# Kernel tuning notes

Measured on AMD Instinct MI355X. Metric: run time of the kernel, lower is better.

## Reference

```python
import jax, jax.numpy as jnp
import numpy as np

N = 100_000      # num nodes
E = 6_400_000    # num edges
P = 12           # periods
F = 32           # output_size (TGCN hidden)


def setup_inputs() -> dict:
    key = jax.random.key(0)
    ks = jax.random.split(key, 16)
    g = lambda i, shape, s=0.1: jax.random.normal(ks[i], shape, dtype=jnp.float32) * s
    zf = jnp.zeros((F,), jnp.float32)
    return {
        "x": jax.random.normal(ks[0], (N, P), dtype=jnp.float32),
        "edge_index": jax.random.randint(ks[1], (2, E), 0, N, dtype=jnp.int64),
        "edge_weight": jax.random.uniform(ks[2], (E,), dtype=jnp.float32),
        "attention": g(3, (P,), 1.0),            # A3TGCN learned period attention
        # GCNConv weights: in_channels=1 -> weight is effectively a length-F vector
        "wc_z": g(4, (F,)), "bc_z": zf,
        "wc_r": g(5, (F,)), "bc_r": zf,
        "wc_h": g(6, (F,)), "bc_h": zf,
        # TGCN gate linears: Linear(2F, F) with bias
        "wl_z": g(7, (2 * F, F)), "bl_z": zf,
        "wl_r": g(8, (2 * F, F)), "bl_r": zf,
        "wl_h": g(9, (2 * F, F)), "bl_h": zf,
        # final Linear(F, 1)
        "w_out": g(10, (F, 1)), "b_out": jnp.zeros((1,), jnp.float32),
    }


def reference(x, edge_index, edge_weight, attention,
              wc_z, bc_z, wc_r, bc_r, wc_h, bc_h,
              wl_z, bl_z, wl_r, bl_r, wl_h, bl_h,
              w_out, b_out):
    n = x.shape[0]
    src, dst = edge_index[0], edge_index[1]

    # GCN normalization with added self-loops (weight 1): D^{-1/2} (A + I) D^{-1/2}
    deg = jax.ops.segment_sum(edge_weight, dst, num_segments=n) + 1.0
    dinv = jax.lax.rsqrt(deg)
    norm = dinv[src] * edge_weight * dinv[dst]          # (E,)

    # GCNConv is linear and in_channels == 1, so conv_g(X_p)_i = agg(X_p)_i * W_g + b_g
    # where agg is the normalized (self-loop augmented) scalar aggregation.
    # Aggregate all periods at once: (E, P) messages -> (N, P)
    agg = jax.ops.segment_sum(norm[:, None] * x[src], dst, num_segments=n)
    agg = agg + (dinv * dinv)[:, None] * x              # self-loop term, (N, P)

    probs = jax.nn.softmax(attention)                   # (P,)
    H0 = jnp.zeros((n, F), x.dtype)                     # A3TGCN calls TGCN with H=None each period
    H_acc = jnp.zeros((n, F), x.dtype)
    for p in range(P):                                  # small fixed structural loop
        s = agg[:, p, None]                             # (N, 1)
        conv_z = s * wc_z + bc_z                        # (N, F)
        conv_r = s * wc_r + bc_r
        conv_h = s * wc_h + bc_h
        Z = jax.nn.sigmoid(jnp.concatenate([conv_z, H0], axis=1) @ wl_z + bl_z)
        R = jax.nn.sigmoid(jnp.concatenate([conv_r, H0], axis=1) @ wl_r + bl_r)
        Ht = jnp.tanh(jnp.concatenate([conv_h, H0 * R], axis=1) @ wl_h + bl_h)
        Hp = Z * H0 + (1.0 - Z) * Ht                    # TGCN single step from zero state
        H_acc = H_acc + probs[p] * Hp

    h = jax.nn.relu(H_acc)
    return h @ w_out + b_out                            # (N, 1)
```

## Files before the change

### kernel.cpp

```cpp
#include <hip/hip_runtime.h>

#define NN 100000
#define EE 6400000
#define PP 12
#define FF 32

#define VV   128
#define BB   782
#define CAP  8832
#define K1B  800
#define CHK  8000
#define AST  13
#define XST  16

__global__ void precompute_k(const float* __restrict__ att,
                             const float* __restrict__ wc_z, const float* __restrict__ bc_z,
                             const float* __restrict__ wc_h, const float* __restrict__ bc_h,
                             const float* __restrict__ wl_z, const float* __restrict__ bl_z,
                             const float* __restrict__ wl_h, const float* __restrict__ bl_h,
                             float* __restrict__ tabs) {
    int j = threadIdx.x;
    if (j < FF) {
        float az = 0.f, cz = 0.f, ah = 0.f, ch = 0.f;
        for (int f = 0; f < FF; ++f) {
            float wz = wl_z[f * FF + j];
            float wh = wl_h[f * FF + j];
            az += wc_z[f] * wz;
            cz += bc_z[f] * wz;
            ah += wc_h[f] * wh;
            ch += bc_h[f] * wh;
        }
        tabs[16 + j]          = az;
        tabs[16 + FF + j]     = cz + bl_z[j];
        tabs[16 + 2 * FF + j] = ah;
        tabs[16 + 3 * FF + j] = ch + bl_h[j];
    } else if (j == FF) {
        float a[PP];
        float m = -1e30f;
        for (int p = 0; p < PP; ++p) { a[p] = att[p]; m = fmaxf(m, a[p]); }
        float s = 0.f;
        for (int p = 0; p < PP; ++p) { a[p] = __expf(a[p] - m); s += a[p]; }
        for (int p = 0; p < PP; ++p) tabs[p] = a[p] / s;
    }
}

__global__ __launch_bounds__(512) void bucket_k(const int* __restrict__ src,
                                                const int* __restrict__ dst,
                                                const float* __restrict__ ew,
                                                int* __restrict__ bucket_cnt,
                                                uint2* __restrict__ recs) {
    __shared__ int hist[BB];
    __shared__ int offs[BB];
    int tid = threadIdx.x;
    int beg = blockIdx.x * CHK;
    int end = beg + CHK;

    for (int b = tid; b < BB; b += 512) hist[b] = 0;
    __syncthreads();

    for (int e = beg + tid; e < end; e += 512)
        atomicAdd(&hist[dst[e] >> 7], 1);
    __syncthreads();

    for (int b = tid; b < BB; b += 512) {
        int h = hist[b];
        offs[b] = h ? atomicAdd(&bucket_cnt[b], h) : 0;
    }
    __syncthreads();

    for (int e = beg + tid; e < end; e += 512) {
        int d = dst[e];
        int bin   = d >> 7;
        int local = d & (VV - 1);
        int o = atomicAdd(&offs[bin], 1);
        if (o < CAP) {
            uint2 r;
            r.x = ((unsigned)local << 17) | (unsigned)src[e];
            r.y = __float_as_uint(ew[e]);
            recs[(size_t)bin * CAP + o] = r;
        }
    }
}

__global__ __launch_bounds__(256) void deg2_k(const int* __restrict__ bucket_cnt,
                                              const uint2* __restrict__ recs,
                                              const float* __restrict__ x,
                                              float* __restrict__ xds) {
    __shared__ unsigned long long wsum[VV];
    int b = blockIdx.x;
    int tid = threadIdx.x;
    if (tid < VV) wsum[tid] = 0ull;
    __syncthreads();

    int n = min(bucket_cnt[b], CAP);
    const uint2* r = recs + (size_t)b * CAP;
    for (int k = tid; k < n; k += 256) {
        uint2 v = r[k];
        unsigned long long w = (unsigned long long)(__uint_as_float(v.y) * 4294967296.0f);
        atomicAdd(&wsum[v.x >> 17], w);
    }
    __syncthreads();

    int node = b * VV + tid;
    if (tid < VV && node < NN) {
        float wf = (float)wsum[tid] * (1.0f / 4294967296.0f);
        float dv = rsqrtf(wf + 1.0f);
        const float4* xr = (const float4*)(x + (size_t)node * PP);
        float4* xo = (float4*)(xds + ((size_t)node << 4));
        #pragma unroll
        for (int q = 0; q < 3; ++q) {
            float4 v = xr[q];
            v.x *= dv; v.y *= dv; v.z *= dv; v.w *= dv;
            xo[q] = v;
        }
        xds[((size_t)node << 4) + 12] = dv;
    }
}

__global__ __launch_bounds__(512) void sortagg_k(const int* __restrict__ bucket_cnt,
                                                 const uint2* __restrict__ recs,
                                                 const float* __restrict__ xds,
                                                 const float* __restrict__ tabs,
                                                 const float* __restrict__ w_out,
                                                 const float* __restrict__ b_out,
                                                 float* __restrict__ out) {
    __shared__ uint2 srec[CAP];
    __shared__ int   h[VV];
    __shared__ int   starts_s[VV];
    __shared__ int   offs[VV];
    __shared__ int   cnts_s[VV];
    __shared__ float agg[VV * AST];
    int b = blockIdx.x;
    int tid = threadIdx.x;

    if (tid < VV) h[tid] = 0;
    __syncthreads();

    int n = min(bucket_cnt[b], CAP);
    const uint2* r = recs + (size_t)b * CAP;

    for (int k = tid; k < n; k += 512)
        atomicAdd(&h[r[k].x >> 17], 1);
    __syncthreads();

    int own = (tid < VV) ? h[tid] : 0;
    #pragma unroll
    for (int off = 1; off < VV; off <<= 1) {
        int t = (tid < VV && tid >= off) ? h[tid - off] : 0;
        __syncthreads();
        if (tid < VV) h[tid] += t;
        __syncthreads();
    }
    if (tid < VV) {
        int pre = h[tid] - own;
        starts_s[tid] = pre;
        offs[tid]     = pre;
        cnts_s[tid]   = own;
    }
    __syncthreads();

    for (int k = tid; k < n; k += 512) {
        uint2 v = r[k];
        int p = atomicAdd(&offs[v.x >> 17], 1);
        srec[p] = v;
    }
    __syncthreads();

    {
        int local = tid >> 2;
        int q     = tid & 3;
        int st = starts_s[local];
        int cn = cnts_s[local];

        float acc[PP];
        #pragma unroll
        for (int p = 0; p < PP; ++p) acc[p] = 0.f;

        for (int m = q; m < cn; m += 4) {
            uint2 v = srec[st + m];
            float c = __uint_as_float(v.y);
            const float4* xs = (const float4*)(xds + ((size_t)(v.x & 0x1FFFFu) << 4));
            float4 v0 = xs[0], v1 = xs[1], v2 = xs[2];
            acc[0] += c * v0.x;  acc[1] += c * v0.y;  acc[2]  += c * v0.z;  acc[3]  += c * v0.w;
            acc[4] += c * v1.x;  acc[5] += c * v1.y;  acc[6]  += c * v1.z;  acc[7]  += c * v1.w;
            acc[8] += c * v2.x;  acc[9] += c * v2.y;  acc[10] += c * v2.z;  acc[11] += c * v2.w;
        }

        #pragma unroll
        for (int p = 0; p < PP; ++p) {
            acc[p] += __shfl_xor(acc[p], 1, 4);
            acc[p] += __shfl_xor(acc[p], 2, 4);
        }
        if (q == 0) {
            float* ap = &agg[local * AST];
            #pragma unroll
            for (int p = 0; p < PP; ++p) ap[p] = acc[p];
        }
    }
    __syncthreads();

    int g = tid >> 5;
    int j = tid & 31;
    float azj = tabs[16 + j];
    float czj = tabs[16 + FF + j];
    float ahj = tabs[16 + 2 * FF + j];
    float chj = tabs[16 + 3 * FF + j];

    for (int nl = g; nl < VV; nl += 16) {
        int i = b * VV + nl;
        if (i >= NN) continue;
        float dv = xds[((size_t)i << 4) + 12];
        const float* ai = &agg[nl * AST];

        float accum = 0.f;
        #pragma unroll
        for (int p = 0; p < PP; ++p) {
            float sp = dv * (ai[p] + xds[((size_t)i << 4) + p]);
            float pr = tabs[p];
            float uz = sp * azj + czj;
            float uh = sp * ahj + chj;
            float one_minus_z = 1.0f / (1.0f + __expf(uz));
            float e2h = __expf(2.0f * uh);
            float th  = 1.0f - 2.0f / (e2h + 1.0f);
            accum += pr * one_minus_z * th;
        }
        float hv = fmaxf(accum, 0.f) * w_out[j];
        #pragma unroll
        for (int off = 16; off > 0; off >>= 1)
            hv += __shfl_xor(hv, off, 32);
        if (j == 0) out[i] = hv + b_out[0];
    }
}

__global__ __launch_bounds__(256) void deg_k(const int* __restrict__ dst,
                                             const float* __restrict__ ew,
                                             float* __restrict__ deg) {
    int stride = gridDim.x * blockDim.x;
    for (int e = blockIdx.x * blockDim.x + threadIdx.x; e < EE; e += stride)
        atomicAdd(&deg[dst[e]], ew[e]);
}

__global__ __launch_bounds__(256) void dinv_self_k(const float* __restrict__ x,
                                                   float* __restrict__ deg,
                                                   float* __restrict__ agg) {
    int i = blockIdx.x * blockDim.x + threadIdx.x;
    if (i >= NN) return;
    float d  = deg[i] + 1.0f;
    float dv = rsqrtf(d);
    deg[i]   = dv;
    float dv2 = dv * dv;
    const float4* xr = (const float4*)(x + (size_t)i * PP);
    float4* ar = (float4*)(agg + (size_t)i * PP);
    #pragma unroll
    for (int q = 0; q < 3; ++q) {
        float4 v = xr[q];
        v.x *= dv2; v.y *= dv2; v.z *= dv2; v.w *= dv2;
        ar[q] = v;
    }
}

__global__ __launch_bounds__(256) void agg_k(const int* __restrict__ src,
                                             const int* __restrict__ dst,
                                             const float* __restrict__ ew,
                                             const float* __restrict__ x,
                                             const float* __restrict__ dinv,
                                             float* __restrict__ agg) {
    int stride = gridDim.x * blockDim.x;
    for (int e = blockIdx.x * blockDim.x + threadIdx.x; e < EE; e += stride) {
        int s = src[e];
        int d = dst[e];
        float nw = dinv[s] * ew[e] * dinv[d];
        const float4* xs = (const float4*)(x + (size_t)s * PP);
        float* ad = agg + (size_t)d * PP;
        float4 v0 = xs[0], v1 = xs[1], v2 = xs[2];
        atomicAdd(&ad[0],  nw * v0.x);
        atomicAdd(&ad[1],  nw * v0.y);
        atomicAdd(&ad[2],  nw * v0.z);
        atomicAdd(&ad[3],  nw * v0.w);
        atomicAdd(&ad[4],  nw * v1.x);
        atomicAdd(&ad[5],  nw * v1.y);
        atomicAdd(&ad[6],  nw * v1.z);
        atomicAdd(&ad[7],  nw * v1.w);
        atomicAdd(&ad[8],  nw * v2.x);
        atomicAdd(&ad[9],  nw * v2.y);
        atomicAdd(&ad[10], nw * v2.z);
        atomicAdd(&ad[11], nw * v2.w);
    }
}

__global__ __launch_bounds__(256) void node_k(const float* __restrict__ agg,
                                              const float* __restrict__ tabs,
                                              const float* __restrict__ w_out,
                                              const float* __restrict__ b_out,
                                              float* __restrict__ out) {
    int t = blockIdx.x * blockDim.x + threadIdx.x;
    int i = t >> 5;
    int j = t & 31;
    if (i >= NN) return;
    float azj = tabs[16 + j];
    float czj = tabs[16 + FF + j];
    float ahj = tabs[16 + 2 * FF + j];
    float chj = tabs[16 + 3 * FF + j];
    float acc = 0.f;
    #pragma unroll
    for (int p = 0; p < PP; ++p) {
        float s  = agg[i * PP + p];
        float pr = tabs[p];
        float uz = s * azj + czj;
        float uh = s * ahj + chj;
        float one_minus_z = 1.0f / (1.0f + __expf(uz));
        float e2h = __expf(2.0f * uh);
        float th  = 1.0f - 2.0f / (e2h + 1.0f);
        acc += pr * one_minus_z * th;
    }
    float h = fmaxf(acc, 0.f) * w_out[j];
    #pragma unroll
    for (int off = 16; off > 0; off >>= 1)
        h += __shfl_xor(h, off, 32);
    if (j == 0) out[i] = h + b_out[0];
}

extern "C" void kernel_launch(void* const* d_in, const int* in_sizes, int n_in,
                              void* d_out, int out_size, void* d_ws, size_t ws_size,
                              hipStream_t stream) {
    const float* x    = (const float*)d_in[0];
    const int*   ei   = (const int*)d_in[1];
    const float* ew   = (const float*)d_in[2];
    const float* att  = (const float*)d_in[3];
    const float* wc_z = (const float*)d_in[4];
    const float* bc_z = (const float*)d_in[5];
    const float* wc_h = (const float*)d_in[8];
    const float* bc_h = (const float*)d_in[9];
    const float* wl_z = (const float*)d_in[10];
    const float* bl_z = (const float*)d_in[11];
    const float* wl_h = (const float*)d_in[14];
    const float* bl_h = (const float*)d_in[15];
    const float* wout = (const float*)d_in[16];
    const float* bout = (const float*)d_in[17];
    float* out = (float*)d_out;

    const int* src = ei;
    const int* dst = ei + EE;

    size_t region  = (size_t)BB * CAP * sizeof(uint2);
    size_t cnt_pad = 3136;
    size_t xds_sz  = (size_t)NN * XST * sizeof(float);
    size_t need    = region + cnt_pad + xds_sz + 4096;

    if (ws_size >= need) {
        uint2* recs       = (uint2*)d_ws;
        int*   bucket_cnt = (int*)((char*)d_ws + region);
        float* xds        = (float*)((char*)d_ws + region + cnt_pad);
        float* tabs       = (float*)((char*)d_ws + region + cnt_pad + xds_sz);

        hipMemsetAsync(bucket_cnt, 0, BB * sizeof(int), stream);
        precompute_k<<<1, 64, 0, stream>>>(att, wc_z, bc_z, wc_h, bc_h, wl_z, bl_z, wl_h, bl_h, tabs);
        bucket_k<<<K1B, 512, 0, stream>>>(src, dst, ew, bucket_cnt, recs);
        deg2_k<<<BB, 256, 0, stream>>>(bucket_cnt, recs, x, xds);
        sortagg_k<<<BB, 512, 0, stream>>>(bucket_cnt, recs, xds, tabs, wout, bout, out);
    } else {
        float* deg  = (float*)d_ws;
        float* agg  = deg + NN;
        float* tabs = agg + (size_t)NN * PP;

        hipMemsetAsync(deg, 0, NN * sizeof(float), stream);
        precompute_k<<<1, 64, 0, stream>>>(att, wc_z, bc_z, wc_h, bc_h, wl_z, bl_z, wl_h, bl_h, tabs);
        deg_k<<<4096, 256, 0, stream>>>(dst, ew, deg);
        dinv_self_k<<<(NN + 255) / 256, 256, 0, stream>>>(x, deg, agg);
        agg_k<<<8192, 256, 0, stream>>>(src, dst, ew, x, deg, agg);
        node_k<<<NN * 32 / 256, 256, 0, stream>>>(agg, tabs, wout, bout, out);
    }
}
```

Before: 420.4 us.

## Sort edge chunks locally in LDS and write contiguously with per-chunk bucket offset table

Each bucketing block now fully sorts its 8000-edge chunk by destination bucket in shared memory and writes it out contiguously, recording per-bucket start offsets in a 16-bit table. This replaces scattered global writes and global atomics on bucket counters. The degree and aggregation kernels then gather each bucket's records from 800 chunk segments using that table, which removes the memset and the capacity-padded region. The cost is fragmented, small-segment reads in the consumer kernels and extra shared memory, and the agg buffer now reuses the srec space.

```diff
diff --git a/kernel.cpp b/kernel.cpp
--- a/kernel.cpp
+++ b/kernel.cpp
@@ -10,6 +10,7 @@
 #define CAP  8832
 #define K1B  800
 #define CHK  8000
+#define NBIN 784
 #define AST  13
 #define XST  16
 
@@ -44,60 +45,87 @@
     }
 }
 
-__global__ __launch_bounds__(512) void bucket_k(const int* __restrict__ src,
-                                                const int* __restrict__ dst,
-                                                const float* __restrict__ ew,
-                                                int* __restrict__ bucket_cnt,
-                                                uint2* __restrict__ recs) {
-    __shared__ int hist[BB];
-    __shared__ int offs[BB];
+__global__ __launch_bounds__(512) void bucketsort_k(const int* __restrict__ src,
+                                                    const int* __restrict__ dst,
+                                                    const float* __restrict__ ew,
+                                                    uint2* __restrict__ recs,
+                                                    unsigned short* __restrict__ T16) {
+    __shared__ uint2 srec[CHK];
+    __shared__ int   hist[NBIN];
+    __shared__ int   offs[NBIN];
     int tid = threadIdx.x;
-    int beg = blockIdx.x * CHK;
-    int end = beg + CHK;
-
-    for (int b = tid; b < BB; b += 512) hist[b] = 0;
-    __syncthreads();
-
-    for (int e = beg + tid; e < end; e += 512)
-        atomicAdd(&hist[dst[e] >> 7], 1);
-    __syncthreads();
-
-    for (int b = tid; b < BB; b += 512) {
-        int h = hist[b];
-        offs[b] = h ? atomicAdd(&bucket_cnt[b], h) : 0;
-    }
-    __syncthreads();
-
-    for (int e = beg + tid; e < end; e += 512) {
-        int d = dst[e];
-        int bin   = d >> 7;
-        int local = d & (VV - 1);
-        int o = atomicAdd(&offs[bin], 1);
-        if (o < CAP) {
-            uint2 r;
-            r.x = ((unsigned)local << 17) | (unsigned)src[e];
-            r.y = __float_as_uint(ew[e]);
-            recs[(size_t)bin * CAP + o] = r;
-        }
-    }
-}
-
-__global__ __launch_bounds__(256) void deg2_k(const int* __restrict__ bucket_cnt,
-                                              const uint2* __restrict__ recs,
+    int blk = blockIdx.x;
+    int beg = blk * CHK;
+
+    for (int b = tid; b < NBIN; b += 512) hist[b] = 0;
+    __syncthreads();
+
+    for (int e = tid; e < CHK; e += 512)
+        atomicAdd(&hist[dst[beg + e] >> 7], 1);
+    __syncthreads();
+
+    int i2   = 512 + tid;
+    int own0 = hist[tid];
+    int own1 = (i2 < NBIN) ? hist[i2] : 0;
+    for (int off = 1; off < NBIN; off <<= 1) {
+        int a0 = (tid >= off) ? hist[tid - off] : 0;
+        int a1 = (i2 < NBIN) ? hist[i2 - off] : 0;
+        __syncthreads();
+        hist[tid] += a0;
+        if (i2 < NBIN) hist[i2] += a1;
+        __syncthreads();
+    }
+    offs[tid] = hist[tid] - own0;
+    if (i2 < NBIN) offs[i2] = hist[i2] - own1;
+    __syncthreads();
+
+    for (int b = tid; b < 783; b += 512)
+        T16[(size_t)b * K1B + blk] = (unsigned short)offs[b];
+    __syncthreads();
+
+    for (int e = tid; e < CHK; e += 512) {
+        int ee = beg + e;
+        int d  = dst[ee];
+        uint2 r;
+        r.x = ((unsigned)(d & (VV - 1)) << 17) | (unsigned)src[ee];
+        r.y = __float_as_uint(ew[ee]);
+        int p = atomicAdd(&offs[d >> 7], 1);
+        srec[p] = r;
+    }
+    __syncthreads();
+
+    uint2* o = recs + (size_t)blk * CHK;
+    for (int k = tid; k < CHK; k += 512)
+        o[k] = srec[k];
+}
+
+__global__ __launch_bounds__(512) void deg2_k(const uint2* __restrict__ recs,
+                                              const unsigned short* __restrict__ T16,
                                               const float* __restrict__ x,
                                               float* __restrict__ xds) {
     __shared__ unsigned long long wsum[VV];
+    __shared__ int rstart[K1B], rcnt[K1B];
     int b = blockIdx.x;
     int tid = threadIdx.x;
+
     if (tid < VV) wsum[tid] = 0ull;
-    __syncthreads();
-
-    int n = min(bucket_cnt[b], CAP);
-    const uint2* r = recs + (size_t)b * CAP;
-    for (int k = tid; k < n; k += 256) {
-        uint2 v = r[k];
-        unsigned long long w = (unsigned long long)(__uint_as_float(v.y) * 4294967296.0f);
-        atomicAdd(&wsum[v.x >> 17], w);
+    for (int k = tid; k < K1B; k += 512) {
+        int s = T16[(size_t)b * K1B + k];
+        int e = T16[(size_t)(b + 1) * K1B + k];
+        rstart[k] = s;
+        rcnt[k]   = e - s;
+    }
+    __syncthreads();
+
+    int wv = tid >> 6, ln = tid & 63;
+    for (int k = wv; k < K1B; k += 8) {
+        int st = rstart[k], cn = rcnt[k];
+        const uint2* rr = recs + (size_t)k * CHK + st;
+        for (int m = ln; m < cn; m += 64) {
+            uint2 v = rr[m];
+            unsigned long long w = (unsigned long long)(__uint_as_float(v.y) * 4294967296.0f);
+            atomicAdd(&wsum[v.x >> 17], w);
+        }
     }
     __syncthreads();
 
@@ -117,30 +145,36 @@
     }
 }
 
-__global__ __launch_bounds__(512) void sortagg_k(const int* __restrict__ bucket_cnt,
-                                                 const uint2* __restrict__ recs,
+__global__ __launch_bounds__(512) void sortagg_k(const uint2* __restrict__ recs,
+                                                 const unsigned short* __restrict__ T16,
                                                  const float* __restrict__ xds,
                                                  const float* __restrict__ tabs,
                                                  const float* __restrict__ w_out,
                                                  const float* __restrict__ b_out,
                                                  float* __restrict__ out) {
     __shared__ uint2 srec[CAP];
-    __shared__ int   h[VV];
-    __shared__ int   starts_s[VV];
-    __shared__ int   offs[VV];
-    __shared__ int   cnts_s[VV];
-    __shared__ float agg[VV * AST];
+    __shared__ int   h[VV], starts_s[VV], offs[VV], cnts_s[VV];
+    __shared__ int   rstart[K1B], rcnt[K1B];
     int b = blockIdx.x;
     int tid = threadIdx.x;
 
     if (tid < VV) h[tid] = 0;
-    __syncthreads();
-
-    int n = min(bucket_cnt[b], CAP);
-    const uint2* r = recs + (size_t)b * CAP;
-
-    for (int k = tid; k < n; k += 512)
-        atomicAdd(&h[r[k].x >> 17], 1);
+    for (int k = tid; k < K1B; k += 512) {
+        int s = T16[(size_t)b * K1B + k];
+        int e = T16[(size_t)(b + 1) * K1B + k];
+        rstart[k] = s;
+        rcnt[k]   = e - s;
+    }
+    __syncthreads();
+
+    int wv = tid >> 6, ln = tid & 63;
+
+    for (int k = wv; k < K1B; k += 8) {
+        int st = rstart[k], cn = rcnt[k];
+        const uint2* rr = recs + (size_t)k * CHK + st;
+        for (int m = ln; m < cn; m += 64)
+            atomicAdd(&h[rr[m].x >> 17], 1);
+    }
     __syncthreads();
 
     int own = (tid < VV) ? h[tid] : 0;
@@ -159,20 +193,25 @@
     }
     __syncthreads();
 
-    for (int k = tid; k < n; k += 512) {
-        uint2 v = r[k];
-        int p = atomicAdd(&offs[v.x >> 17], 1);
-        srec[p] = v;
-    }
-    __syncthreads();
-
+    for (int k = wv; k < K1B; k += 8) {
+        int st = rstart[k], cn = rcnt[k];
+        const uint2* rr = recs + (size_t)k * CHK + st;
+        for (int m = ln; m < cn; m += 64) {
+            uint2 v = rr[m];
+            int p = atomicAdd(&offs[v.x >> 17], 1);
+            if (p < CAP) srec[p] = v;
+        }
+    }
+    __syncthreads();
+
+    float acc[PP];
     {
         int local = tid >> 2;
         int q     = tid & 3;
-        int st = starts_s[local];
-        int cn = cnts_s[local];
-
-        float acc[PP];
+        int st = min(starts_s[local], CAP);
+        int en = min(starts_s[local] + cnts_s[local], CAP);
+        int cn = en - st;
+
         #pragma unroll
         for (int p = 0; p < PP; ++p) acc[p] = 0.f;
 
@@ -191,11 +230,14 @@
             acc[p] += __shfl_xor(acc[p], 1, 4);
             acc[p] += __shfl_xor(acc[p], 2, 4);
         }
-        if (q == 0) {
-            float* ap = &agg[local * AST];
-            #pragma unroll
-            for (int p = 0; p < PP; ++p) ap[p] = acc[p];
-        }
+    }
+    __syncthreads();
+
+    float* agg = (float*)srec;
+    if ((tid & 3) == 0) {
+        float* ap = &agg[(tid >> 2) * AST];
+        #pragma unroll
+        for (int p = 0; p < PP; ++p) ap[p] = acc[p];
     }
     __syncthreads();
 
@@ -342,22 +384,21 @@
     const int* src = ei;
     const int* dst = ei + EE;
 
-    size_t region  = (size_t)BB * CAP * sizeof(uint2);
-    size_t cnt_pad = 3136;
-    size_t xds_sz  = (size_t)NN * XST * sizeof(float);
-    size_t need    = region + cnt_pad + xds_sz + 4096;
+    size_t region = (size_t)EE * sizeof(uint2);
+    size_t tbl_sz = (size_t)783 * K1B * sizeof(unsigned short);
+    size_t xds_sz = (size_t)NN * XST * sizeof(float);
+    size_t need   = region + tbl_sz + xds_sz + 4096;
 
     if (ws_size >= need) {
-        uint2* recs       = (uint2*)d_ws;
-        int*   bucket_cnt = (int*)((char*)d_ws + region);
-        float* xds        = (float*)((char*)d_ws + region + cnt_pad);
-        float* tabs       = (float*)((char*)d_ws + region + cnt_pad + xds_sz);
-
-        hipMemsetAsync(bucket_cnt, 0, BB * sizeof(int), stream);
+        uint2*          recs = (uint2*)d_ws;
+        unsigned short* T16  = (unsigned short*)((char*)d_ws + region);
+        float*          xds  = (float*)((char*)d_ws + region + tbl_sz);
+        float*          tabs = (float*)((char*)d_ws + region + tbl_sz + xds_sz);
+
         precompute_k<<<1, 64, 0, stream>>>(att, wc_z, bc_z, wc_h, bc_h, wl_z, bl_z, wl_h, bl_h, tabs);
-        bucket_k<<<K1B, 512, 0, stream>>>(src, dst, ew, bucket_cnt, recs);
-        deg2_k<<<BB, 256, 0, stream>>>(bucket_cnt, recs, x, xds);
-        sortagg_k<<<BB, 512, 0, stream>>>(bucket_cnt, recs, xds, tabs, wout, bout, out);
+        bucketsort_k<<<K1B, 512, 0, stream>>>(src, dst, ew, recs, T16);
+        deg2_k<<<BB, 512, 0, stream>>>(recs, T16, x, xds);
+        sortagg_k<<<BB, 512, 0, stream>>>(recs, T16, xds, tabs, wout, bout, out);
     } else {
         float* deg  = (float*)d_ws;
         float* agg  = deg + NN;
```

Result: slower. 502.8 us (+19.6%).
